# Performance work log

Hardware: AMD Instinct MI355X
Metric: run time of the kernel (lower is better)

The kernel has to match this reference:

```python
import jax, jax.numpy as jnp
import numpy as np

B, C, N, K, D = 4, 64, 40960, 16, 128
EPS = 1e-5  # BatchNorm2d default eps


def _bn_relu(x, g, b, m, v):
    # inference BN over channel axis 1, then ReLU (pt_utils.Conv2d default activation)
    scale = g / jnp.sqrt(v + EPS)
    shift = b - m * scale
    return jax.nn.relu(x * scale[None, :, None, None] + shift[None, :, None, None])


def setup_inputs() -> dict:
    key = jax.random.key(0)
    ks = jax.random.split(key, 16)
    feature = jax.random.normal(ks[0], (B, C, N, 1), jnp.float32)
    neigh_idx = jax.random.randint(ks[1], (B, N, K), 0, N)
    w1 = jax.random.normal(ks[2], (C, C), jnp.float32) * 0.05
    w2 = jax.random.normal(ks[3], (D, C), jnp.float32) * 0.05
    w3 = jax.random.normal(ks[4], (D, C), jnp.float32) * 0.05
    def bn(kg, km, kv, n):
        g = 1.0 + 0.1 * jax.random.normal(kg, (n,), jnp.float32)
        b = 0.1 * jax.random.normal(km, (n,), jnp.float32)
        m = 0.1 * jax.random.normal(kv, (n,), jnp.float32)
        v = jax.random.uniform(jax.random.fold_in(kv, 1), (n,), jnp.float32, 0.5, 1.5)
        return g, b, m, v
    g1, b1, m1, v1 = bn(ks[5], ks[6], ks[7], C)
    g2, b2, m2, v2 = bn(ks[8], ks[9], ks[10], D)
    g3, b3, m3, v3 = bn(ks[11], ks[12], ks[13], D)
    return dict(feature=feature, neigh_idx=neigh_idx,
                w1=w1, g1=g1, b1=b1, m1=m1, v1=v1,
                w2=w2, g2=g2, b2=b2, m2=m2, v2=v2,
                w3=w3, g3=g3, b3=b3, m3=m3, v3=v3)


def reference(feature, neigh_idx, w1, g1, b1, m1, v1, w2, g2, b2, m2, v2,
              w3, g3, b3, m3, v3):
    # gather_neighbour: feature [B,C,N,1], neigh_idx [B,N,K] -> [B,C,N,K]
    f = feature[:, :, :, 0]                                   # [B,C,N]
    f_neigh = jax.vmap(lambda fb, ib: fb[:, ib])(f, neigh_idx)  # [B,C,N,K]
    # mlp1: 1x1 conv + BN + ReLU
    h = jnp.einsum('oc,bcnk->bonk', w1, f_neigh)
    h = _bn_relu(h, g1, b1, m1, v1)
    # sum over neighbors
    h = jnp.sum(h, axis=-1, keepdims=True)                    # [B,C,N,1]
    # mlp2
    h = jnp.einsum('oc,bcnk->bonk', w2, h)
    h = _bn_relu(h, g2, b2, m2, v2)
    # mlp3 on original feature (residual branch)
    s = jnp.einsum('oc,bcnk->bonk', w3, feature)
    s = _bn_relu(s, g3, b3, m3, v3)
    return h + s                                              # [B,D,N,1]
```

## Files before the change

kernel.cpp:

```cpp
#include <hip/hip_runtime.h>

#define EPSV 1e-5f
constexpr int Bb = 4, Cc = 64, Nn = 40960, Kk = 16, Dd = 128;
constexpr int G = 5;
constexpr int TPB = Nn / 16;

typedef float f32x4 __attribute__((ext_vector_type(4)));
typedef __bf16 bf16x8 __attribute__((ext_vector_type(8)));
typedef unsigned short us8 __attribute__((ext_vector_type(8)));
typedef unsigned short us4 __attribute__((ext_vector_type(4)));

__device__ inline unsigned short f2bf(float x) {
    unsigned u = __builtin_bit_cast(unsigned, x);
    u += 0x7FFFu + ((u >> 16) & 1u);
    return (unsigned short)(u >> 16);
}

__global__ __launch_bounds__(256) void prep_weights(
    const float* __restrict__ w1, const float* __restrict__ g1, const float* __restrict__ b1,
    const float* __restrict__ m1, const float* __restrict__ v1,
    const float* __restrict__ w2, const float* __restrict__ g2, const float* __restrict__ b2,
    const float* __restrict__ m2, const float* __restrict__ v2,
    const float* __restrict__ w3, const float* __restrict__ g3, const float* __restrict__ b3,
    const float* __restrict__ m3, const float* __restrict__ v3,
    unsigned short* __restrict__ w1s, unsigned short* __restrict__ w2s, unsigned short* __restrict__ w3s,
    float* __restrict__ sh1, float* __restrict__ sh2, float* __restrict__ sh3) {
    const int e = blockIdx.x * 256 + threadIdx.x;
    if (e < 4096) {
        const int o = e >> 6;
        const float sc = g1[o] * rsqrtf(v1[o] + EPSV);
        w1s[e] = f2bf(w1[e] * sc);
    } else if (e < 12288) {
        const int i = e - 4096, o = i >> 6;
        const float sc = g2[o] * rsqrtf(v2[o] + EPSV);
        w2s[i] = f2bf(w2[i] * sc);
    } else if (e < 20480) {
        const int i = e - 12288, o = i >> 6;
        const float sc = g3[o] * rsqrtf(v3[o] + EPSV);
        w3s[i] = f2bf(w3[i] * sc);
    }
    if (e < 64) sh1[e] = b1[e] - m1[e] * (g1[e] * rsqrtf(v1[e] + EPSV));
    else if (e < 192) { const int d = e - 64;  sh2[d] = b2[d] - m2[d] * (g2[d] * rsqrtf(v2[d] + EPSV)); }
    else if (e < 320) { const int d = e - 192; sh3[d] = b3[d] - m3[d] * (g3[d] * rsqrtf(v3[d] + EPSV)); }
}

__global__ __launch_bounds__(256) void passA(const float* __restrict__ f,
                                             const unsigned short* __restrict__ w1s,
                                             unsigned short* __restrict__ G1) {
    __shared__ float s[64 * 65];
    __shared__ __attribute__((aligned(16))) unsigned short sg1[64 * 72];

    const int tid = threadIdx.x, w = tid >> 6, lane = tid & 63;
    const int c15 = lane & 15, q = lane >> 4;
    const int b = blockIdx.x / 640;
    const int n0 = (blockIdx.x % 640) * 64;

    const float* src = f + ((size_t)b * Cc + w * 16) * Nn + n0 + lane;
#pragma unroll
    for (int i = 0; i < 16; ++i) s[(w * 16 + i) * 65 + lane] = src[(size_t)i * Nn];

    const int o1 = w * 16 + c15;
    bf16x8 bw1[2];
#pragma unroll
    for (int ks = 0; ks < 2; ++ks)
        bw1[ks] = __builtin_bit_cast(bf16x8, *(const uint4*)(w1s + o1 * 64 + ks * 32 + q * 8));
    __syncthreads();

#pragma unroll
    for (int mt = 0; mt < 4; ++mt) {
        const int pt = mt * 16 + c15;
        us8 A0, A1;
#pragma unroll
        for (int j = 0; j < 8; ++j) A0[j] = f2bf(s[(q * 8 + j) * 65 + pt]);
#pragma unroll
        for (int j = 0; j < 8; ++j) A1[j] = f2bf(s[(32 + q * 8 + j) * 65 + pt]);
        f32x4 g = {0.f, 0.f, 0.f, 0.f};
        g = __builtin_amdgcn_mfma_f32_16x16x32_bf16(__builtin_bit_cast(bf16x8, A0), bw1[0], g, 0, 0, 0);
        g = __builtin_amdgcn_mfma_f32_16x16x32_bf16(__builtin_bit_cast(bf16x8, A1), bw1[1], g, 0, 0, 0);
#pragma unroll
        for (int r = 0; r < 4; ++r) sg1[(mt * 16 + q * 4 + r) * 72 + o1] = f2bf(g[r]);
    }
    __syncthreads();

    {
        const int p = tid >> 2, ck = tid & 3;
        const uint4 v0 = *(const uint4*)(sg1 + p * 72 + ck * 16);
        const uint4 v1 = *(const uint4*)(sg1 + p * 72 + ck * 16 + 8);
        unsigned short* dst = G1 + ((size_t)b * Nn + n0 + p) * 64 + ck * 16;
        *(uint4*)dst = v0;
        *(uint4*)(dst + 8) = v1;
    }
}

__global__ __launch_bounds__(256, 4) void passB(
    const unsigned short* __restrict__ G1, const float* __restrict__ f,
    const int* __restrict__ idx,
    const unsigned short* __restrict__ w2s, const unsigned short* __restrict__ w3s,
    const float* __restrict__ sh1, const float* __restrict__ sh2, const float* __restrict__ sh3,
    float* __restrict__ out) {
    __shared__ __attribute__((aligned(16))) unsigned short s_h1[16 * 72];
    __shared__ float s_out[16 * 132];

    const int tid  = threadIdx.x;
    const int wave = tid >> 6;
    const int lane = tid & 63;
    const int c15  = lane & 15;
    const int q    = lane >> 4;
    const int pg   = tid >> 4;
    const int cg   = tid & 15;

    const int t0  = blockIdx.x * G;
    const int b   = t0 / TPB;
    const int nb0 = (t0 - b * TPB) * 16;

    float sh2v[2], sh3v[2];
    bf16x8 bw2[2][2], bw3[2][2];
#pragma unroll
    for (int nt = 0; nt < 2; ++nt) {
        const int d = wave * 32 + nt * 16 + c15;
        sh2v[nt] = sh2[d];
        sh3v[nt] = sh3[d];
#pragma unroll
        for (int ks = 0; ks < 2; ++ks) {
            bw2[nt][ks] = __builtin_bit_cast(bf16x8, *(const uint4*)(w2s + d * 64 + ks * 32 + q * 8));
            bw3[nt][ks] = __builtin_bit_cast(bf16x8, *(const uint4*)(w3s + d * 64 + ks * 32 + q * 8));
        }
    }
    float shA[4];
#pragma unroll
    for (int j = 0; j < 4; ++j) shA[j] = sh1[cg * 4 + j];

    const unsigned short* G1b = G1 + (size_t)b * Nn * 64;
    const float* fb0 = f + (size_t)b * Cc * Nn;

    for (int g = 0; g < G; ++g) {
        const int n0 = nb0 + g * 16;

        const float* fown = fb0 + n0 + c15;
        us8 F0, F1;
#pragma unroll
        for (int j = 0; j < 8; ++j) F0[j] = f2bf(fown[(size_t)(q * 8 + j) * Nn]);
#pragma unroll
        for (int j = 0; j < 8; ++j) F1[j] = f2bf(fown[(size_t)(32 + q * 8 + j) * Nn]);

        const int myidx = idx[((size_t)b * Nn + n0) * Kk + tid];

        float a0 = 0.f, a1 = 0.f, a2 = 0.f, a3 = 0.f;
#pragma unroll
        for (int k = 0; k < 16; ++k) {
            const int nb = __shfl(myidx, (pg & 3) * 16 + k, 64);
            const uint2 d2 = *(const uint2*)(G1b + (size_t)nb * 64 + cg * 4);
            const float f0 = __builtin_bit_cast(float, d2.x << 16);
            const float f1 = __builtin_bit_cast(float, d2.x & 0xffff0000u);
            const float f2v = __builtin_bit_cast(float, d2.y << 16);
            const float f3 = __builtin_bit_cast(float, d2.y & 0xffff0000u);
            a0 += fmaxf(f0 + shA[0], 0.f);
            a1 += fmaxf(f1 + shA[1], 0.f);
            a2 += fmaxf(f2v + shA[2], 0.f);
            a3 += fmaxf(f3 + shA[3], 0.f);
        }

        __syncthreads();
        us4 hv;
        hv[0] = f2bf(a0); hv[1] = f2bf(a1); hv[2] = f2bf(a2); hv[3] = f2bf(a3);
        *(us4*)(s_h1 + pg * 72 + cg * 4) = hv;
        __syncthreads();

        const unsigned short* h1row = s_h1 + c15 * 72;
        const bf16x8 ah0 = __builtin_bit_cast(bf16x8, *(const uint4*)(h1row + q * 8));
        const bf16x8 ah1 = __builtin_bit_cast(bf16x8, *(const uint4*)(h1row + 32 + q * 8));
        const bf16x8 af0 = __builtin_bit_cast(bf16x8, F0);
        const bf16x8 af1 = __builtin_bit_cast(bf16x8, F1);

#pragma unroll
        for (int nt = 0; nt < 2; ++nt) {
            f32x4 h2 = {sh2v[nt], sh2v[nt], sh2v[nt], sh2v[nt]};
            f32x4 s3 = {sh3v[nt], sh3v[nt], sh3v[nt], sh3v[nt]};
            h2 = __builtin_amdgcn_mfma_f32_16x16x32_bf16(ah0, bw2[nt][0], h2, 0, 0, 0);
            h2 = __builtin_amdgcn_mfma_f32_16x16x32_bf16(ah1, bw2[nt][1], h2, 0, 0, 0);
            s3 = __builtin_amdgcn_mfma_f32_16x16x32_bf16(af0, bw3[nt][0], s3, 0, 0, 0);
            s3 = __builtin_amdgcn_mfma_f32_16x16x32_bf16(af1, bw3[nt][1], s3, 0, 0, 0);
            const int d = wave * 32 + nt * 16 + c15;
#pragma unroll
            for (int r = 0; r < 4; ++r) {
                const int p = q * 4 + r;
                s_out[p * 132 + d] = fmaxf(h2[r], 0.f) + fmaxf(s3[r], 0.f);
            }
        }
        __syncthreads();

        {
            const int d = tid >> 1, half = tid & 1;
            float v[8];
#pragma unroll
            for (int i = 0; i < 8; ++i) v[i] = s_out[(half * 8 + i) * 132 + d];
            float* dst = out + ((size_t)b * Dd + d) * Nn + n0 + half * 8;
            __builtin_nontemporal_store((f32x4){v[0], v[1], v[2], v[3]}, (f32x4*)dst);
            __builtin_nontemporal_store((f32x4){v[4], v[5], v[6], v[7]}, (f32x4*)(dst + 4));
        }
    }
}

extern "C" void kernel_launch(void* const* d_in, const int* in_sizes, int n_in,
                              void* d_out, int out_size, void* d_ws, size_t ws_size,
                              hipStream_t stream) {
    const float* feature = (const float*)d_in[0];
    const int*   neigh   = (const int*)d_in[1];
    const float* w1 = (const float*)d_in[2];
    const float* g1 = (const float*)d_in[3];
    const float* b1 = (const float*)d_in[4];
    const float* m1 = (const float*)d_in[5];
    const float* v1 = (const float*)d_in[6];
    const float* w2 = (const float*)d_in[7];
    const float* g2 = (const float*)d_in[8];
    const float* b2 = (const float*)d_in[9];
    const float* m2 = (const float*)d_in[10];
    const float* v2 = (const float*)d_in[11];
    const float* w3 = (const float*)d_in[12];
    const float* g3 = (const float*)d_in[13];
    const float* b3 = (const float*)d_in[14];
    const float* m3 = (const float*)d_in[15];
    const float* v3 = (const float*)d_in[16];
    float* out = (float*)d_out;

    char* ws = (char*)d_ws;
    unsigned short* G1  = (unsigned short*)ws;
    unsigned short* w1s = (unsigned short*)(ws + 20971520);
    unsigned short* w2s = (unsigned short*)(ws + 20971520 + 8192);
    unsigned short* w3s = (unsigned short*)(ws + 20971520 + 24576);
    float* sh1 = (float*)(ws + 20971520 + 40960);
    float* sh2 = (float*)(ws + 20971520 + 41216);
    float* sh3 = (float*)(ws + 20971520 + 41728);

    prep_weights<<<80, 256, 0, stream>>>(w1, g1, b1, m1, v1, w2, g2, b2, m2, v2,
                                         w3, g3, b3, m3, v3, w1s, w2s, w3s, sh1, sh2, sh3);
    passA<<<Bb * 640, 256, 0, stream>>>(feature, w1s, G1);
    passB<<<(Bb * TPB) / G, 256, 0, stream>>>(G1, feature, neigh, w2s, w3s,
                                              sh1, sh2, sh3, out);
}
```

Baseline: 228.6 us.

## Precompute BN1+ReLU in passA and restructure passB to two tiles per block

Moves the BN1 shift and ReLU into passA so the stored G1 already holds activated values, which removes per-neighbour add/max work in the gather loop. passB now handles two 16-point tiles per block with both tiles' neighbour gathers issued together to raise memory-level parallelism. It also writes 32-point contiguous output rows and raises the occupancy hint to 6 blocks. The trade-off is more blocks and a larger shared output buffer. Rounding ReLU outputs to bf16 before summing differs slightly from the original order.

```diff
diff --git a/kernel.cpp b/kernel.cpp
--- a/kernel.cpp
+++ b/kernel.cpp
@@ -2,8 +2,8 @@
 
 #define EPSV 1e-5f
 constexpr int Bb = 4, Cc = 64, Nn = 40960, Kk = 16, Dd = 128;
-constexpr int G = 5;
 constexpr int TPB = Nn / 16;
+constexpr int PPB = TPB / 2;
 
 typedef float f32x4 __attribute__((ext_vector_type(4)));
 typedef __bf16 bf16x8 __attribute__((ext_vector_type(8)));
@@ -46,6 +46,7 @@
 
 __global__ __launch_bounds__(256) void passA(const float* __restrict__ f,
                                              const unsigned short* __restrict__ w1s,
+                                             const float* __restrict__ sh1,
                                              unsigned short* __restrict__ G1) {
     __shared__ float s[64 * 65];
     __shared__ __attribute__((aligned(16))) unsigned short sg1[64 * 72];
@@ -60,6 +61,7 @@
     for (int i = 0; i < 16; ++i) s[(w * 16 + i) * 65 + lane] = src[(size_t)i * Nn];
 
     const int o1 = w * 16 + c15;
+    const float sh1v = sh1[o1];
     bf16x8 bw1[2];
 #pragma unroll
     for (int ks = 0; ks < 2; ++ks)
@@ -78,7 +80,8 @@
         g = __builtin_amdgcn_mfma_f32_16x16x32_bf16(__builtin_bit_cast(bf16x8, A0), bw1[0], g, 0, 0, 0);
         g = __builtin_amdgcn_mfma_f32_16x16x32_bf16(__builtin_bit_cast(bf16x8, A1), bw1[1], g, 0, 0, 0);
 #pragma unroll
-        for (int r = 0; r < 4; ++r) sg1[(mt * 16 + q * 4 + r) * 72 + o1] = f2bf(g[r]);
+        for (int r = 0; r < 4; ++r)
+            sg1[(mt * 16 + q * 4 + r) * 72 + o1] = f2bf(fmaxf(g[r] + sh1v, 0.f));
     }
     __syncthreads();
 
@@ -92,14 +95,14 @@
     }
 }
 
-__global__ __launch_bounds__(256, 4) void passB(
+__global__ __launch_bounds__(256, 6) void passB(
     const unsigned short* __restrict__ G1, const float* __restrict__ f,
     const int* __restrict__ idx,
     const unsigned short* __restrict__ w2s, const unsigned short* __restrict__ w3s,
-    const float* __restrict__ sh1, const float* __restrict__ sh2, const float* __restrict__ sh3,
+    const float* __restrict__ sh2, const float* __restrict__ sh3,
     float* __restrict__ out) {
     __shared__ __attribute__((aligned(16))) unsigned short s_h1[16 * 72];
-    __shared__ float s_out[16 * 132];
+    __shared__ float s_out[32 * 133];
 
     const int tid  = threadIdx.x;
     const int wave = tid >> 6;
@@ -109,9 +112,16 @@
     const int pg   = tid >> 4;
     const int cg   = tid & 15;
 
-    const int t0  = blockIdx.x * G;
-    const int b   = t0 / TPB;
-    const int nb0 = (t0 - b * TPB) * 16;
+    const int pr = blockIdx.x;
+    const int b  = pr / PPB;
+    const int n0 = (pr - b * PPB) * 32;
+
+    const unsigned short* G1b = G1 + (size_t)b * Nn * 64;
+    const float* fb0 = f + (size_t)b * Cc * Nn;
+
+    const int* idxp = idx + ((size_t)b * Nn + n0) * Kk;
+    const int myidxA = idxp[tid];
+    const int myidxB = idxp[256 + tid];
 
     float sh2v[2], sh3v[2];
     bf16x8 bw2[2][2], bw3[2][2];
@@ -126,52 +136,48 @@
             bw3[nt][ks] = __builtin_bit_cast(bf16x8, *(const uint4*)(w3s + d * 64 + ks * 32 + q * 8));
         }
     }
-    float shA[4];
-#pragma unroll
-    for (int j = 0; j < 4; ++j) shA[j] = sh1[cg * 4 + j];
-
-    const unsigned short* G1b = G1 + (size_t)b * Nn * 64;
-    const float* fb0 = f + (size_t)b * Cc * Nn;
-
-    for (int g = 0; g < G; ++g) {
-        const int n0 = nb0 + g * 16;
-
+
+    us8 FA0, FA1;
+    {
         const float* fown = fb0 + n0 + c15;
-        us8 F0, F1;
-#pragma unroll
-        for (int j = 0; j < 8; ++j) F0[j] = f2bf(fown[(size_t)(q * 8 + j) * Nn]);
-#pragma unroll
-        for (int j = 0; j < 8; ++j) F1[j] = f2bf(fown[(size_t)(32 + q * 8 + j) * Nn]);
-
-        const int myidx = idx[((size_t)b * Nn + n0) * Kk + tid];
-
-        float a0 = 0.f, a1 = 0.f, a2 = 0.f, a3 = 0.f;
-#pragma unroll
-        for (int k = 0; k < 16; ++k) {
-            const int nb = __shfl(myidx, (pg & 3) * 16 + k, 64);
-            const uint2 d2 = *(const uint2*)(G1b + (size_t)nb * 64 + cg * 4);
-            const float f0 = __builtin_bit_cast(float, d2.x << 16);
-            const float f1 = __builtin_bit_cast(float, d2.x & 0xffff0000u);
-            const float f2v = __builtin_bit_cast(float, d2.y << 16);
-            const float f3 = __builtin_bit_cast(float, d2.y & 0xffff0000u);
-            a0 += fmaxf(f0 + shA[0], 0.f);
-            a1 += fmaxf(f1 + shA[1], 0.f);
-            a2 += fmaxf(f2v + shA[2], 0.f);
-            a3 += fmaxf(f3 + shA[3], 0.f);
-        }
-
-        __syncthreads();
+#pragma unroll
+        for (int j = 0; j < 8; ++j) FA0[j] = f2bf(fown[(size_t)(q * 8 + j) * Nn]);
+#pragma unroll
+        for (int j = 0; j < 8; ++j) FA1[j] = f2bf(fown[(size_t)(32 + q * 8 + j) * Nn]);
+    }
+
+    float aA0 = 0.f, aA1 = 0.f, aA2 = 0.f, aA3 = 0.f;
+    float aB0 = 0.f, aB1 = 0.f, aB2 = 0.f, aB3 = 0.f;
+#pragma unroll
+    for (int k = 0; k < 16; ++k) {
+        const int la  = (pg & 3) * 16 + k;
+        const int nbA = __shfl(myidxA, la, 64);
+        const int nbB = __shfl(myidxB, la, 64);
+        const uint2 dA = *(const uint2*)(G1b + (size_t)nbA * 64 + cg * 4);
+        const uint2 dB = *(const uint2*)(G1b + (size_t)nbB * 64 + cg * 4);
+        aA0 += __builtin_bit_cast(float, dA.x << 16);
+        aA1 += __builtin_bit_cast(float, dA.x & 0xffff0000u);
+        aA2 += __builtin_bit_cast(float, dA.y << 16);
+        aA3 += __builtin_bit_cast(float, dA.y & 0xffff0000u);
+        aB0 += __builtin_bit_cast(float, dB.x << 16);
+        aB1 += __builtin_bit_cast(float, dB.x & 0xffff0000u);
+        aB2 += __builtin_bit_cast(float, dB.y << 16);
+        aB3 += __builtin_bit_cast(float, dB.y & 0xffff0000u);
+    }
+
+    {
         us4 hv;
-        hv[0] = f2bf(a0); hv[1] = f2bf(a1); hv[2] = f2bf(a2); hv[3] = f2bf(a3);
+        hv[0] = f2bf(aA0); hv[1] = f2bf(aA1); hv[2] = f2bf(aA2); hv[3] = f2bf(aA3);
         *(us4*)(s_h1 + pg * 72 + cg * 4) = hv;
-        __syncthreads();
-
+    }
+    __syncthreads();
+
+    {
         const unsigned short* h1row = s_h1 + c15 * 72;
         const bf16x8 ah0 = __builtin_bit_cast(bf16x8, *(const uint4*)(h1row + q * 8));
         const bf16x8 ah1 = __builtin_bit_cast(bf16x8, *(const uint4*)(h1row + 32 + q * 8));
-        const bf16x8 af0 = __builtin_bit_cast(bf16x8, F0);
-        const bf16x8 af1 = __builtin_bit_cast(bf16x8, F1);
-
+        const bf16x8 af0 = __builtin_bit_cast(bf16x8, FA0);
+        const bf16x8 af1 = __builtin_bit_cast(bf16x8, FA1);
 #pragma unroll
         for (int nt = 0; nt < 2; ++nt) {
             f32x4 h2 = {sh2v[nt], sh2v[nt], sh2v[nt], sh2v[nt]};
@@ -182,21 +188,59 @@
             s3 = __builtin_amdgcn_mfma_f32_16x16x32_bf16(af1, bw3[nt][1], s3, 0, 0, 0);
             const int d = wave * 32 + nt * 16 + c15;
 #pragma unroll
-            for (int r = 0; r < 4; ++r) {
-                const int p = q * 4 + r;
-                s_out[p * 132 + d] = fmaxf(h2[r], 0.f) + fmaxf(s3[r], 0.f);
-            }
-        }
-        __syncthreads();
-
-        {
-            const int d = tid >> 1, half = tid & 1;
-            float v[8];
-#pragma unroll
-            for (int i = 0; i < 8; ++i) v[i] = s_out[(half * 8 + i) * 132 + d];
-            float* dst = out + ((size_t)b * Dd + d) * Nn + n0 + half * 8;
-            __builtin_nontemporal_store((f32x4){v[0], v[1], v[2], v[3]}, (f32x4*)dst);
-            __builtin_nontemporal_store((f32x4){v[4], v[5], v[6], v[7]}, (f32x4*)(dst + 4));
+            for (int r = 0; r < 4; ++r)
+                s_out[(q * 4 + r) * 133 + d] = fmaxf(h2[r], 0.f) + fmaxf(s3[r], 0.f);
+        }
+    }
+    __syncthreads();
+
+    us8 FB0, FB1;
+    {
+        const float* fown = fb0 + n0 + 16 + c15;
+#pragma unroll
+        for (int j = 0; j < 8; ++j) FB0[j] = f2bf(fown[(size_t)(q * 8 + j) * Nn]);
+#pragma unroll
+        for (int j = 0; j < 8; ++j) FB1[j] = f2bf(fown[(size_t)(32 + q * 8 + j) * Nn]);
+    }
+    {
+        us4 hv;
+        hv[0] = f2bf(aB0); hv[1] = f2bf(aB1); hv[2] = f2bf(aB2); hv[3] = f2bf(aB3);
+        *(us4*)(s_h1 + pg * 72 + cg * 4) = hv;
+    }
+    __syncthreads();
+
+    {
+        const unsigned short* h1row = s_h1 + c15 * 72;
+        const bf16x8 ah0 = __builtin_bit_cast(bf16x8, *(const uint4*)(h1row + q * 8));
+        const bf16x8 ah1 = __builtin_bit_cast(bf16x8, *(const uint4*)(h1row + 32 + q * 8));
+        const bf16x8 af0 = __builtin_bit_cast(bf16x8, FB0);
+        const bf16x8 af1 = __builtin_bit_cast(bf16x8, FB1);
+#pragma unroll
+        for (int nt = 0; nt < 2; ++nt) {
+            f32x4 h2 = {sh2v[nt], sh2v[nt], sh2v[nt], sh2v[nt]};
+            f32x4 s3 = {sh3v[nt], sh3v[nt], sh3v[nt], sh3v[nt]};
+            h2 = __builtin_amdgcn_mfma_f32_16x16x32_bf16(ah0, bw2[nt][0], h2, 0, 0, 0);
+            h2 = __builtin_amdgcn_mfma_f32_16x16x32_bf16(ah1, bw2[nt][1], h2, 0, 0, 0);
+            s3 = __builtin_amdgcn_mfma_f32_16x16x32_bf16(af0, bw3[nt][0], s3, 0, 0, 0);
+            s3 = __builtin_amdgcn_mfma_f32_16x16x32_bf16(af1, bw3[nt][1], s3, 0, 0, 0);
+            const int d = wave * 32 + nt * 16 + c15;
+#pragma unroll
+            for (int r = 0; r < 4; ++r)
+                s_out[(16 + q * 4 + r) * 133 + d] = fmaxf(h2[r], 0.f) + fmaxf(s3[r], 0.f);
+        }
+    }
+    __syncthreads();
+
+    {
+        const int dd = tid >> 3;
+        const int ck = tid & 7;
+#pragma unroll
+        for (int r4 = 0; r4 < 4; ++r4) {
+            const int d = r4 * 32 + dd;
+            f32x4 v;
+#pragma unroll
+            for (int i = 0; i < 4; ++i) v[i] = s_out[(ck * 4 + i) * 133 + d];
+            __builtin_nontemporal_store(v, (f32x4*)(out + ((size_t)b * Dd + d) * Nn + n0 + ck * 4));
         }
     }
 }
@@ -234,7 +278,7 @@
 
     prep_weights<<<80, 256, 0, stream>>>(w1, g1, b1, m1, v1, w2, g2, b2, m2, v2,
                                          w3, g3, b3, m3, v3, w1s, w2s, w3s, sh1, sh2, sh3);
-    passA<<<Bb * 640, 256, 0, stream>>>(feature, w1s, G1);
-    passB<<<(Bb * TPB) / G, 256, 0, stream>>>(G1, feature, neigh, w2s, w3s,
-                                              sh1, sh2, sh3, out);
-}
+    passA<<<Bb * 640, 256, 0, stream>>>(feature, w1s, sh1, G1);
+    passB<<<Bb * PPB, 256, 0, stream>>>(G1, feature, neigh, w2s, w3s,
+                                        sh2, sh3, out);
+}
```

Result: slower. 375.5 us (+64.2%).

## Move BN1+ReLU into passA, prefetch indices, and batch output stores over two groups

Applied to the files above, without the earlier changes.

Applies the mlp1 shift and ReLU once per point in passA before writing the bf16 G1 table, rather than once per gathered neighbour in passB, so the gather loop only accumulates. passB now prefetches the next group's neighbour indices during the current group's gather. Output is staged across two 16-point groups so each row writes 32 contiguous floats per store phase, and G drops from 5 to 4 to keep an even group count. The padded staging buffer grows to 32x133 floats. Rounding the post-ReLU values to bf16 before summing changes numerics slightly.

```diff
diff --git a/kernel.cpp b/kernel.cpp
--- a/kernel.cpp
+++ b/kernel.cpp
@@ -2,7 +2,7 @@
 
 #define EPSV 1e-5f
 constexpr int Bb = 4, Cc = 64, Nn = 40960, Kk = 16, Dd = 128;
-constexpr int G = 5;
+constexpr int G = 4;
 constexpr int TPB = Nn / 16;
 
 typedef float f32x4 __attribute__((ext_vector_type(4)));
@@ -46,6 +46,7 @@
 
 __global__ __launch_bounds__(256) void passA(const float* __restrict__ f,
                                              const unsigned short* __restrict__ w1s,
+                                             const float* __restrict__ sh1,
                                              unsigned short* __restrict__ G1) {
     __shared__ float s[64 * 65];
     __shared__ __attribute__((aligned(16))) unsigned short sg1[64 * 72];
@@ -60,6 +61,7 @@
     for (int i = 0; i < 16; ++i) s[(w * 16 + i) * 65 + lane] = src[(size_t)i * Nn];
 
     const int o1 = w * 16 + c15;
+    const float sh1v = sh1[o1];
     bf16x8 bw1[2];
 #pragma unroll
     for (int ks = 0; ks < 2; ++ks)
@@ -78,7 +80,8 @@
         g = __builtin_amdgcn_mfma_f32_16x16x32_bf16(__builtin_bit_cast(bf16x8, A0), bw1[0], g, 0, 0, 0);
         g = __builtin_amdgcn_mfma_f32_16x16x32_bf16(__builtin_bit_cast(bf16x8, A1), bw1[1], g, 0, 0, 0);
 #pragma unroll
-        for (int r = 0; r < 4; ++r) sg1[(mt * 16 + q * 4 + r) * 72 + o1] = f2bf(g[r]);
+        for (int r = 0; r < 4; ++r)
+            sg1[(mt * 16 + q * 4 + r) * 72 + o1] = f2bf(fmaxf(g[r] + sh1v, 0.f));
     }
     __syncthreads();
 
@@ -96,10 +99,10 @@
     const unsigned short* __restrict__ G1, const float* __restrict__ f,
     const int* __restrict__ idx,
     const unsigned short* __restrict__ w2s, const unsigned short* __restrict__ w3s,
-    const float* __restrict__ sh1, const float* __restrict__ sh2, const float* __restrict__ sh3,
+    const float* __restrict__ sh2, const float* __restrict__ sh3,
     float* __restrict__ out) {
     __shared__ __attribute__((aligned(16))) unsigned short s_h1[16 * 72];
-    __shared__ float s_out[16 * 132];
+    __shared__ float s_out[32 * 133];
 
     const int tid  = threadIdx.x;
     const int wave = tid >> 6;
@@ -126,39 +129,36 @@
             bw3[nt][ks] = __builtin_bit_cast(bf16x8, *(const uint4*)(w3s + d * 64 + ks * 32 + q * 8));
         }
     }
-    float shA[4];
-#pragma unroll
-    for (int j = 0; j < 4; ++j) shA[j] = sh1[cg * 4 + j];
 
     const unsigned short* G1b = G1 + (size_t)b * Nn * 64;
     const float* fb0 = f + (size_t)b * Cc * Nn;
+    const int* idxp = idx + ((size_t)b * Nn + nb0) * Kk;
+
+    int myidx = idxp[tid];
 
     for (int g = 0; g < G; ++g) {
         const int n0 = nb0 + g * 16;
 
+        const int myidxN = (g + 1 < G) ? idxp[(g + 1) * 256 + tid] : 0;
+
         const float* fown = fb0 + n0 + c15;
         us8 F0, F1;
 #pragma unroll
         for (int j = 0; j < 8; ++j) F0[j] = f2bf(fown[(size_t)(q * 8 + j) * Nn]);
 #pragma unroll
         for (int j = 0; j < 8; ++j) F1[j] = f2bf(fown[(size_t)(32 + q * 8 + j) * Nn]);
-
-        const int myidx = idx[((size_t)b * Nn + n0) * Kk + tid];
 
         float a0 = 0.f, a1 = 0.f, a2 = 0.f, a3 = 0.f;
 #pragma unroll
         for (int k = 0; k < 16; ++k) {
             const int nb = __shfl(myidx, (pg & 3) * 16 + k, 64);
             const uint2 d2 = *(const uint2*)(G1b + (size_t)nb * 64 + cg * 4);
-            const float f0 = __builtin_bit_cast(float, d2.x << 16);
-            const float f1 = __builtin_bit_cast(float, d2.x & 0xffff0000u);
-            const float f2v = __builtin_bit_cast(float, d2.y << 16);
-            const float f3 = __builtin_bit_cast(float, d2.y & 0xffff0000u);
-            a0 += fmaxf(f0 + shA[0], 0.f);
-            a1 += fmaxf(f1 + shA[1], 0.f);
-            a2 += fmaxf(f2v + shA[2], 0.f);
-            a3 += fmaxf(f3 + shA[3], 0.f);
-        }
+            a0 += __builtin_bit_cast(float, d2.x << 16);
+            a1 += __builtin_bit_cast(float, d2.x & 0xffff0000u);
+            a2 += __builtin_bit_cast(float, d2.y << 16);
+            a3 += __builtin_bit_cast(float, d2.y & 0xffff0000u);
+        }
+        myidx = myidxN;
 
         __syncthreads();
         us4 hv;
@@ -172,6 +172,7 @@
         const bf16x8 af0 = __builtin_bit_cast(bf16x8, F0);
         const bf16x8 af1 = __builtin_bit_cast(bf16x8, F1);
 
+        const int prow = (g & 1) * 16;
 #pragma unroll
         for (int nt = 0; nt < 2; ++nt) {
             f32x4 h2 = {sh2v[nt], sh2v[nt], sh2v[nt], sh2v[nt]};
@@ -182,21 +183,23 @@
             s3 = __builtin_amdgcn_mfma_f32_16x16x32_bf16(af1, bw3[nt][1], s3, 0, 0, 0);
             const int d = wave * 32 + nt * 16 + c15;
 #pragma unroll
-            for (int r = 0; r < 4; ++r) {
-                const int p = q * 4 + r;
-                s_out[p * 132 + d] = fmaxf(h2[r], 0.f) + fmaxf(s3[r], 0.f);
+            for (int r = 0; r < 4; ++r)
+                s_out[(prow + q * 4 + r) * 133 + d] = fmaxf(h2[r], 0.f) + fmaxf(s3[r], 0.f);
+        }
+        __syncthreads();
+
+        if (g & 1) {
+            const int np = n0 - 16;
+            const int dd = tid >> 3;
+            const int ck = tid & 7;
+#pragma unroll
+            for (int r4 = 0; r4 < 4; ++r4) {
+                const int d = r4 * 32 + dd;
+                f32x4 v;
+#pragma unroll
+                for (int i = 0; i < 4; ++i) v[i] = s_out[(ck * 4 + i) * 133 + d];
+                __builtin_nontemporal_store(v, (f32x4*)(out + ((size_t)b * Dd + d) * Nn + np + ck * 4));
             }
-        }
-        __syncthreads();
-
-        {
-            const int d = tid >> 1, half = tid & 1;
-            float v[8];
-#pragma unroll
-            for (int i = 0; i < 8; ++i) v[i] = s_out[(half * 8 + i) * 132 + d];
-            float* dst = out + ((size_t)b * Dd + d) * Nn + n0 + half * 8;
-            __builtin_nontemporal_store((f32x4){v[0], v[1], v[2], v[3]}, (f32x4*)dst);
-            __builtin_nontemporal_store((f32x4){v[4], v[5], v[6], v[7]}, (f32x4*)(dst + 4));
         }
     }
 }
@@ -234,7 +237,7 @@
 
     prep_weights<<<80, 256, 0, stream>>>(w1, g1, b1, m1, v1, w2, g2, b2, m2, v2,
                                          w3, g3, b3, m3, v3, w1s, w2s, w3s, sh1, sh2, sh3);
-    passA<<<Bb * 640, 256, 0, stream>>>(feature, w1s, G1);
+    passA<<<Bb * 640, 256, 0, stream>>>(feature, w1s, sh1, G1);
     passB<<<(Bb * TPB) / G, 256, 0, stream>>>(G1, feature, neigh, w2s, w3s,
-                                              sh1, sh2, sh3, out);
-}
+                                              sh2, sh3, out);
+}
```

After: 214.4 us. -6.2%, faster.
